# Optimization experiments

Measured on AMD Instinct MI355X. Metric: run time of the kernel, lower is better.

The kernel has to match this reference:

```python
import jax, jax.numpy as jnp
import numpy as np

B, N, D, OUT = 8, 65536, 128, 256
PARENT_IDX, BLOCK_START = 6, 7
relu = jax.nn.relu

def _w(key, fi, fo):
    return jax.random.normal(key, (fi, fo), dtype=jnp.float32) / np.sqrt(fi).astype(np.float32)

def setup_inputs() -> dict:
    key = jax.random.key(0)
    ks = jax.random.split(key, 16)
    feat = jax.random.normal(ks[0], (B, N, 6), dtype=jnp.float32)
    # parent index of each node, local to its batch's node axis
    pidx = jax.random.randint(ks[1], (B, N), 0, N).astype(jnp.float32)
    # block_start == 1 marks root nodes (parent feature is zeroed there)
    root = jnp.zeros((B, N), jnp.float32).at[:, 0].set(1.0)
    data = jnp.concatenate([feat, pidx[..., None], root[..., None]], axis=-1)
    z = lambda d: jnp.zeros((d,), jnp.float32)
    return {
        'data': data,
        'W1_0': _w(ks[2], 6, D),     'b1_0': z(D), 'W1_1': _w(ks[3], D, D), 'b1_1': z(D),
        'W2_0': _w(ks[4], 2 * D, D), 'b2_0': z(D), 'W2_1': _w(ks[5], D, D), 'b2_1': z(D),
        'W3_0': _w(ks[6], 2 * D, D), 'b3_0': z(D), 'W3_1': _w(ks[7], D, D), 'b3_1': z(D),
        'W4_0': _w(ks[8], 2 * D, D), 'b4_0': z(D), 'W4_1': _w(ks[9], D, D), 'b4_1': z(D),
        'Wfc': _w(ks[10], D, OUT),   'bfc': z(OUT),
    }

def reference(data, W1_0, b1_0, W1_1, b1_1, W2_0, b2_0, W2_1, b2_1,
              W3_0, b3_0, W3_1, b3_1, W4_0, b4_0, W4_1, b4_1, Wfc, bfc):
    pidx = jax.lax.stop_gradient(data[..., PARENT_IDX]).astype(jnp.int32)  # [B,N]
    root = jax.lax.stop_gradient(data[..., BLOCK_START]) == 1.0            # [B,N]

    def gather_parent(f):
        # [B,N,D] -> parent-node features, hard-coded to 0 at root nodes
        p = jnp.take_along_axis(f, pidx[:, :, None], axis=1)
        return jnp.where(root[:, :, None], 0.0, p)

    def res_block(f, W0, b0, W1, b1):
        h = jnp.concatenate([f, gather_parent(f)], axis=-1)  # [B,N,2D]
        h = relu(h @ W0 + b0) @ W1 + b1                      # mlp_dolastrelu=False
        return relu(h + f)

    x = data[..., :6]                        # ind_keep for in_feat_len == 6
    f1 = relu(x @ W1_0 + b1_0) @ W1_1 + b1_1 # nodewise_mlp1
    f2 = res_block(f1, W2_0, b2_0, W2_1, b2_1)
    f3 = res_block(f2, W3_0, b3_0, W3_1, b3_1)
    f4 = res_block(f3, W4_0, b4_0, W4_1, b4_1)
    return f4 @ Wfc + bfc                    # [B,N,256] occupancy logits
```

## Files before the change

kernel.cpp:

```cpp
#include <hip/hip_runtime.h>
#include <hip/hip_bf16.h>


typedef __bf16 bf16;
typedef bf16 bf16x8 __attribute__((ext_vector_type(8)));
typedef bf16 bf16x4 __attribute__((ext_vector_type(4)));
typedef float f32x4 __attribute__((ext_vector_type(4)));

#define MFMA16(a, b, c) __builtin_amdgcn_mfma_f32_16x16x32_bf16((a), (b), (c), 0, 0, 0)

#define BAR_LGKM() asm volatile("s_waitcnt lgkmcnt(0)\ns_barrier" ::: "memory")
#define BAR_VM(N) asm volatile("s_waitcnt vmcnt(" #N ")\ns_barrier" ::: "memory")

#define ZB    0
#define W10T  128
#define W11T  4224
#define W20T  20608
#define W21T  53376
#define W30T  69760
#define W31T  102528
#define W40T  118912
#define W41T  151680
#define WFCT  168064
#define PREP_TOTAL 200832
#define FA_BYTE  524288
#define F_STRIDE 134221824
#define FB_BYTE  (FA_BYTE + F_STRIDE)
#define PT_BYTE  (FA_BYTE + 2 * F_STRIDE)
#define ZROW_IDX 524288

__device__ __forceinline__ void gload16(const void* g, void* l) {
  __builtin_amdgcn_global_load_lds(
      (__attribute__((address_space(1))) void*)(g),
      (__attribute__((address_space(3))) void*)(l), 16, 0, 0);
}

__global__ void prep_kernel(const float* __restrict__ W1_0, const float* __restrict__ W1_1,
                            const float* __restrict__ W2_0, const float* __restrict__ W2_1,
                            const float* __restrict__ W3_0, const float* __restrict__ W3_1,
                            const float* __restrict__ W4_0, const float* __restrict__ W4_1,
                            const float* __restrict__ Wfc, bf16* __restrict__ wsb) {
  int i = blockIdx.x * 256 + threadIdx.x;
  if (i < 128) { wsb[ZB + i] = (bf16)0.0f; return; }
  i -= 128;
  if (i < 4096) { int n = i >> 5, k = i & 31;
    wsb[W10T + i] = (bf16)((k < 6) ? W1_0[k * 128 + n] : 0.0f); return; }
  i -= 4096;
  if (i < 16384) { int n = i >> 7, k = i & 127; wsb[W11T + i] = (bf16)W1_1[k * 128 + n]; return; }
  i -= 16384;
  if (i < 32768) { int n = i >> 8, k = i & 255; wsb[W20T + i] = (bf16)W2_0[k * 128 + n]; return; }
  i -= 32768;
  if (i < 16384) { int n = i >> 7, k = i & 127; wsb[W21T + i] = (bf16)W2_1[k * 128 + n]; return; }
  i -= 16384;
  if (i < 32768) { int n = i >> 8, k = i & 255; wsb[W30T + i] = (bf16)W3_0[k * 128 + n]; return; }
  i -= 32768;
  if (i < 16384) { int n = i >> 7, k = i & 127; wsb[W31T + i] = (bf16)W3_1[k * 128 + n]; return; }
  i -= 16384;
  if (i < 32768) { int n = i >> 8, k = i & 255; wsb[W40T + i] = (bf16)W4_0[k * 128 + n]; return; }
  i -= 32768;
  if (i < 16384) { int n = i >> 7, k = i & 127; wsb[W41T + i] = (bf16)W4_1[k * 128 + n]; return; }
  i -= 16384;
  if (i < 32768) { int n = i >> 7, k = i & 127; wsb[WFCT + i] = (bf16)Wfc[k * 256 + n]; return; }
}

__global__ void pidx_kernel(const float* __restrict__ data, int* __restrict__ partab,
                            bf16* __restrict__ fA, bf16* __restrict__ fB) {
  int m = blockIdx.x * 256 + threadIdx.x;
  float2 pr = *(const float2*)(data + (long)m * 8 + 6);
  partab[m] = (pr.y == 1.0f) ? ZROW_IDX : ((m & ~65535) + (int)pr.x);
  if (m < 128) {
    fA[(long)ZROW_IDX * 128 + m] = (bf16)0.0f;
    fB[(long)ZROW_IDX * 128 + m] = (bf16)0.0f;
  }
}

__device__ __forceinline__ void stage_tile(const bf16* __restrict__ f_in,
                                           const int* __restrict__ partab, long mt0,
                                           char* dst, int tid) {
  const int wv = tid >> 6;
  int par[8];
#pragma unroll
  for (int r = 0; r < 8; ++r) par[r] = partab[mt0 + r * 8 + (tid >> 5)];
#pragma unroll
  for (int r = 0; r < 8; ++r) {
    int row = r * 8 + (tid >> 5);
    int gp = tid & 31;
    int g = (gp & 8) | ((gp & 7) ^ (row & 7));
    const bf16* base = (gp < 16) ? (f_in + (mt0 + row) * 128) : (f_in + (long)par[r] * 128);
    gload16(base + g * 8, dst + (r * 256 + wv * 64) * 16);
  }
}

__device__ __forceinline__ void stage_ftile(const bf16* __restrict__ f_in, long mt0,
                                            char* dst, int tid) {
  const int wv = tid >> 6;
#pragma unroll
  for (int r = 0; r < 4; ++r) {
    int G = r * 256 + tid, row = G >> 4, gl = G & 15;
    int g = (gl & 8) | ((gl & 7) ^ (row & 7));
    gload16(f_in + (mt0 + row) * 128 + g * 8, dst + (r * 256 + wv * 64) * 16);
  }
}

__global__ __launch_bounds__(256, 3) void stage1_kernel(
    const float* __restrict__ data, const bf16* __restrict__ w0t, const float* __restrict__ b0,
    const bf16* __restrict__ w1t, const float* __restrict__ b1, bf16* __restrict__ f_out) {
  __shared__ alignas(128) char Hb[2][16384];

  const int tid = threadIdx.x;
  const int lane = tid & 63, wv = tid >> 6;
  const int lr = lane & 15, lq = lane >> 4;
  const long brow = (long)blockIdx.x * 512;
  const int n0 = wv * 32;

  bf16x8 w0f[2];
#pragma unroll
  for (int nf = 0; nf < 2; ++nf)
    w0f[nf] = *(const bf16x8*)(w0t + (long)(n0 + nf * 16 + lr) * 32 + lq * 8);
  bf16x8 w1f[4][2];
#pragma unroll
  for (int kc = 0; kc < 4; ++kc)
#pragma unroll
    for (int nf = 0; nf < 2; ++nf)
      w1f[kc][nf] = *(const bf16x8*)(w1t + (long)(n0 + nf * 16 + lr) * 128 + kc * 32 + lq * 8);
  f32x4 b0v[2], b1v[2];
#pragma unroll
  for (int nf = 0; nf < 2; ++nf) {
    b0v[nf] = *(const f32x4*)(b0 + n0 + nf * 16 + lq * 4);
    b1v[nf] = *(const f32x4*)(b1 + n0 + nf * 16 + lq * 4);
  }

  float4 xlo[4], xhi[4];
  if (lq == 0) {
#pragma unroll
    for (int mf = 0; mf < 4; ++mf) {
      const float* dp = data + (brow + mf * 16 + lr) * 8;
      xlo[mf] = *(const float4*)dp;
      xhi[mf] = *(const float4*)(dp + 4);
    }
  }

#pragma unroll 1
  for (int t = 0; t < 8; ++t) {
    bf16x8 xa[4];
#pragma unroll
    for (int mf = 0; mf < 4; ++mf) {
#pragma unroll
      for (int j = 0; j < 8; ++j) xa[mf][j] = (bf16)0.0f;
      if (lq == 0) {
#pragma unroll
        for (int j = 0; j < 4; ++j) xa[mf][j] = (bf16)xlo[mf][j];
        xa[mf][4] = (bf16)xhi[mf][0];
        xa[mf][5] = (bf16)xhi[mf][1];
      }
    }
    if (lq == 0) {
      long nb = brow + (long)((t < 7) ? t + 1 : 7) * 64;
#pragma unroll
      for (int mf = 0; mf < 4; ++mf) {
        const float* dp = data + (nb + mf * 16 + lr) * 8;
        xlo[mf] = *(const float4*)dp;
        xhi[mf] = *(const float4*)(dp + 4);
      }
    }

    f32x4 acc[4][2];
#pragma unroll
    for (int mf = 0; mf < 4; ++mf)
#pragma unroll
      for (int nf = 0; nf < 2; ++nf) acc[mf][nf] = b0v[nf];
#pragma unroll
    for (int mf = 0; mf < 4; ++mf)
#pragma unroll
      for (int nf = 0; nf < 2; ++nf) acc[mf][nf] = MFMA16(w0f[nf], xa[mf], acc[mf][nf]);

    char* H = Hb[t & 1];
#pragma unroll
    for (int mf = 0; mf < 4; ++mf)
#pragma unroll
      for (int nf = 0; nf < 2; ++nf) {
        int row = mf * 16 + lr, nc = n0 + nf * 16 + lq * 4;
        bf16x4 p;
#pragma unroll
        for (int j = 0; j < 4; ++j) p[j] = (bf16)fmaxf(acc[mf][nf][j], 0.0f);
        int g = nc >> 3, gp = (g & 8) | ((g & 7) ^ (row & 7));
        *(bf16x4*)(H + row * 256 + gp * 16 + (nc & 7) * 2) = p;
      }
    BAR_LGKM();

    f32x4 acc2[4][2];
#pragma unroll
    for (int mf = 0; mf < 4; ++mf)
#pragma unroll
      for (int nf = 0; nf < 2; ++nf) acc2[mf][nf] = b1v[nf];
#pragma unroll
    for (int kc = 0; kc < 4; ++kc) {
      bf16x8 a[4];
#pragma unroll
      for (int mf = 0; mf < 4; ++mf) {
        int row = mf * 16 + lr, g = kc * 4 + lq;
        int gp = (g & 8) | ((g & 7) ^ (row & 7));
        a[mf] = *(const bf16x8*)(H + row * 256 + gp * 16);
      }
#pragma unroll
      for (int mf = 0; mf < 4; ++mf)
#pragma unroll
        for (int nf = 0; nf < 2; ++nf) acc2[mf][nf] = MFMA16(w1f[kc][nf], a[mf], acc2[mf][nf]);
    }
    BAR_LGKM();

#pragma unroll
    for (int mf = 0; mf < 4; ++mf)
#pragma unroll
      for (int nf = 0; nf < 2; ++nf) {
        int row = mf * 16 + lr, nc = n0 + nf * 16 + lq * 4;
        bf16x4 p;
#pragma unroll
        for (int j = 0; j < 4; ++j) p[j] = (bf16)acc2[mf][nf][j];
        int g = nc >> 3, gp = (g & 8) | ((g & 7) ^ (row & 7));
        *(bf16x4*)(H + row * 256 + gp * 16 + (nc & 7) * 2) = p;
      }
    BAR_LGKM();

    long mt0 = brow + (long)t * 64;
#pragma unroll
    for (int r = 0; r < 4; ++r) {
      int G = r * 256 + tid, row = G >> 4, gl = G & 15;
      int gp = (gl & 8) | ((gl & 7) ^ (row & 7));
      bf16x8 v = *(const bf16x8*)(H + row * 256 + gp * 16);
      *(bf16x8*)(f_out + (mt0 + row) * 128 + gl * 8) = v;
    }
  }
}

__global__ __launch_bounds__(256, 2) void resblock_kernel(
    const bf16* __restrict__ f_in, const bf16* __restrict__ w0t, const float* __restrict__ b0,
    const bf16* __restrict__ w1t, const float* __restrict__ b1,
    const int* __restrict__ partab, bf16* __restrict__ f_out) {
  __shared__ alignas(128) char At[2][32768];

  const int tid = threadIdx.x;
  const int lane = tid & 63, wv = tid >> 6;
  const int lr = lane & 15, lq = lane >> 4;
  const long brow = (long)blockIdx.x * 1024;
  const int n0 = wv * 32;

  bf16x8 w0f[8][2];
#pragma unroll
  for (int kc = 0; kc < 8; ++kc)
#pragma unroll
    for (int nf = 0; nf < 2; ++nf)
      w0f[kc][nf] = *(const bf16x8*)(w0t + (long)(n0 + nf * 16 + lr) * 256 + kc * 32 + lq * 8);
  bf16x8 w1f[4][2];
#pragma unroll
  for (int kc = 0; kc < 4; ++kc)
#pragma unroll
    for (int nf = 0; nf < 2; ++nf)
      w1f[kc][nf] = *(const bf16x8*)(w1t + (long)(n0 + nf * 16 + lr) * 128 + kc * 32 + lq * 8);
  f32x4 b0v[2], b1v[2];
#pragma unroll
  for (int nf = 0; nf < 2; ++nf) {
    b0v[nf] = *(const f32x4*)(b0 + n0 + nf * 16 + lq * 4);
    b1v[nf] = *(const f32x4*)(b1 + n0 + nf * 16 + lq * 4);
  }

  stage_tile(f_in, partab, brow, At[0], tid);

#pragma unroll 1
  for (int t = 0; t < 16; ++t) {
    stage_tile(f_in, partab, brow + (long)((t < 15) ? t + 1 : 15) * 64, At[(t + 1) & 1], tid);
    if (t == 0) { BAR_VM(16); } else { BAR_VM(20); }
    char* A = At[t & 1];

    f32x4 acc[4][2];
#pragma unroll
    for (int mf = 0; mf < 4; ++mf)
#pragma unroll
      for (int nf = 0; nf < 2; ++nf) acc[mf][nf] = b0v[nf];
#pragma unroll
    for (int kc = 0; kc < 8; ++kc) {
      bf16x8 a[4];
#pragma unroll
      for (int mf = 0; mf < 4; ++mf) {
        int row = mf * 16 + lr, g = kc * 4 + lq;
        int gp = (g & 24) | ((g & 7) ^ (row & 7));
        a[mf] = *(const bf16x8*)(A + row * 512 + gp * 16);
      }
#pragma unroll
      for (int mf = 0; mf < 4; ++mf)
#pragma unroll
        for (int nf = 0; nf < 2; ++nf) acc[mf][nf] = MFMA16(w0f[kc][nf], a[mf], acc[mf][nf]);
    }
    BAR_LGKM();

#pragma unroll
    for (int mf = 0; mf < 4; ++mf)
#pragma unroll
      for (int nf = 0; nf < 2; ++nf) {
        int row = mf * 16 + lr, nc = n0 + nf * 16 + lq * 4;
        bf16x4 p;
#pragma unroll
        for (int j = 0; j < 4; ++j) p[j] = (bf16)fmaxf(acc[mf][nf][j], 0.0f);
        int g = nc >> 3, gp = (g & 8) | ((g & 7) ^ (row & 7));
        *(bf16x4*)(A + row * 512 + 256 + gp * 16 + (nc & 7) * 2) = p;
      }
    f32x4 acc2[4][2];
#pragma unroll
    for (int mf = 0; mf < 4; ++mf)
#pragma unroll
      for (int nf = 0; nf < 2; ++nf) {
        int row = mf * 16 + lr, nc = n0 + nf * 16 + lq * 4;
        int g = nc >> 3, gp = (g & 8) | ((g & 7) ^ (row & 7));
        bf16x4 res = *(const bf16x4*)(A + row * 512 + gp * 16 + (nc & 7) * 2);
#pragma unroll
        for (int j = 0; j < 4; ++j) acc2[mf][nf][j] = b1v[nf][j] + (float)res[j];
      }
    BAR_LGKM();

#pragma unroll
    for (int kc = 0; kc < 4; ++kc) {
      bf16x8 a[4];
#pragma unroll
      for (int mf = 0; mf < 4; ++mf) {
        int row = mf * 16 + lr, g = kc * 4 + lq;
        int gp = (g & 8) | ((g & 7) ^ (row & 7));
        a[mf] = *(const bf16x8*)(A + row * 512 + 256 + gp * 16);
      }
#pragma unroll
      for (int mf = 0; mf < 4; ++mf)
#pragma unroll
        for (int nf = 0; nf < 2; ++nf) acc2[mf][nf] = MFMA16(w1f[kc][nf], a[mf], acc2[mf][nf]);
    }
#pragma unroll
    for (int mf = 0; mf < 4; ++mf)
#pragma unroll
      for (int nf = 0; nf < 2; ++nf) {
        int row = mf * 16 + lr, nc = n0 + nf * 16 + lq * 4;
        bf16x4 p;
#pragma unroll
        for (int j = 0; j < 4; ++j) p[j] = (bf16)fmaxf(acc2[mf][nf][j], 0.0f);
        int g = nc >> 3, gp = (g & 8) | ((g & 7) ^ (row & 7));
        *(bf16x4*)(A + row * 512 + gp * 16 + (nc & 7) * 2) = p;
      }
    BAR_LGKM();

    bf16x8 v[4];
#pragma unroll
    for (int r = 0; r < 4; ++r) {
      int G = r * 256 + tid, row = G >> 4, gl = G & 15;
      int gp = (gl & 8) | ((gl & 7) ^ (row & 7));
      v[r] = *(const bf16x8*)(A + row * 512 + gp * 16);
    }
    BAR_LGKM();
    long mt0 = brow + (long)t * 64;
#pragma unroll
    for (int r = 0; r < 4; ++r) {
      int G = r * 256 + tid, row = G >> 4, gl = G & 15;
      *(bf16x8*)(f_out + (mt0 + row) * 128 + gl * 8) = v[r];
    }
  }
}

__global__ __launch_bounds__(256, 2) void fc_kernel(
    const bf16* __restrict__ f_in, const bf16* __restrict__ wt,
    const float* __restrict__ bias, float* __restrict__ out) {
  __shared__ alignas(128) char Ft[2][16384];

  const int tid = threadIdx.x;
  const int lane = tid & 63, wv = tid >> 6;
  const int lr = lane & 15, lq = lane >> 4;
  const long brow = (long)blockIdx.x * 512;
  const int c0 = wv * 64;

  bf16x8 wf[4][4];
#pragma unroll
  for (int kc = 0; kc < 4; ++kc)
#pragma unroll
    for (int nf = 0; nf < 4; ++nf)
      wf[kc][nf] = *(const bf16x8*)(wt + (long)(c0 + nf * 16 + lr) * 128 + kc * 32 + lq * 8);
  f32x4 bv[4];
#pragma unroll
  for (int nf = 0; nf < 4; ++nf) bv[nf] = *(const f32x4*)(bias + c0 + nf * 16 + lq * 4);

  stage_ftile(f_in, brow, Ft[0], tid);

#pragma unroll 1
  for (int t = 0; t < 8; ++t) {
    stage_ftile(f_in, brow + (long)((t < 7) ? t + 1 : 7) * 64, Ft[(t + 1) & 1], tid);
    if (t == 0) { BAR_VM(4); } else { BAR_VM(20); }
    char* F = Ft[t & 1];

    f32x4 acc[4][4];
#pragma unroll
    for (int mf = 0; mf < 4; ++mf)
#pragma unroll
      for (int nf = 0; nf < 4; ++nf) acc[mf][nf] = bv[nf];
#pragma unroll
    for (int kc = 0; kc < 4; ++kc) {
      bf16x8 a[4];
#pragma unroll
      for (int mf = 0; mf < 4; ++mf) {
        int row = mf * 16 + lr, g = kc * 4 + lq;
        int gp = (g & 8) | ((g & 7) ^ (row & 7));
        a[mf] = *(const bf16x8*)(F + row * 256 + gp * 16);
      }
#pragma unroll
      for (int mf = 0; mf < 4; ++mf)
#pragma unroll
        for (int nf = 0; nf < 4; ++nf) acc[mf][nf] = MFMA16(wf[kc][nf], a[mf], acc[mf][nf]);
    }
    BAR_LGKM();

    long mt0 = brow + (long)t * 64;
#pragma unroll
    for (int mf = 0; mf < 4; ++mf)
#pragma unroll
      for (int nf = 0; nf < 4; ++nf) {
        long row = mt0 + mf * 16 + lr;
        int col = c0 + nf * 16 + lq * 4;
        *(f32x4*)(out + row * 256 + col) = acc[mf][nf];
      }
  }
}

extern "C" void kernel_launch(void* const* d_in, const int* in_sizes, int n_in,
                              void* d_out, int out_size, void* d_ws, size_t ws_size,
                              hipStream_t stream) {
  const float* data = (const float*)d_in[0];
  const float* W1_0 = (const float*)d_in[1];
  const float* b1_0 = (const float*)d_in[2];
  const float* W1_1 = (const float*)d_in[3];
  const float* b1_1 = (const float*)d_in[4];
  const float* W2_0 = (const float*)d_in[5];
  const float* b2_0 = (const float*)d_in[6];
  const float* W2_1 = (const float*)d_in[7];
  const float* b2_1 = (const float*)d_in[8];
  const float* W3_0 = (const float*)d_in[9];
  const float* b3_0 = (const float*)d_in[10];
  const float* W3_1 = (const float*)d_in[11];
  const float* b3_1 = (const float*)d_in[12];
  const float* W4_0 = (const float*)d_in[13];
  const float* b4_0 = (const float*)d_in[14];
  const float* W4_1 = (const float*)d_in[15];
  const float* b4_1 = (const float*)d_in[16];
  const float* Wfc = (const float*)d_in[17];
  const float* bfc = (const float*)d_in[18];

  bf16* wsb = (bf16*)d_ws;
  bf16* fA = (bf16*)((char*)d_ws + FA_BYTE);
  bf16* fB = (bf16*)((char*)d_ws + FB_BYTE);
  int* partab = (int*)((char*)d_ws + PT_BYTE);

  prep_kernel<<<(PREP_TOTAL + 255) / 256, 256, 0, stream>>>(W1_0, W1_1, W2_0, W2_1, W3_0, W3_1,
                                                            W4_0, W4_1, Wfc, wsb);
  pidx_kernel<<<2048, 256, 0, stream>>>(data, partab, fA, fB);
  stage1_kernel<<<1024, 256, 0, stream>>>(data, wsb + W10T, b1_0, wsb + W11T, b1_1, fA);
  resblock_kernel<<<512, 256, 0, stream>>>(fA, wsb + W20T, b2_0, wsb + W21T, b2_1, partab, fB);
  resblock_kernel<<<512, 256, 0, stream>>>(fB, wsb + W30T, b3_0, wsb + W31T, b3_1, partab, fA);
  resblock_kernel<<<512, 256, 0, stream>>>(fA, wsb + W40T, b4_0, wsb + W41T, b4_1, partab, fB);
  fc_kernel<<<1024, 256, 0, stream>>>(fB, wsb + WFCT, bfc, (float*)d_out);
}
```

Measured before the change: 427.5 us.

## Fuse final FC projection into last residual block kernel

The last residual block now takes a template flag that makes it run the 128->256 output projection directly from the bf16 tile held in shared memory and write fp32 logits, instead of storing f4 to global memory and launching a separate FC kernel. This removes one kernel launch and the global write and reread of the final feature map. In exchange, the fused kernel reloads FC weight fragments from global/L2 for every tile in two halves to limit register pressure. The wait count on the async-load barrier is also changed to account for the different outstanding load pattern.

After: 512.0 us. 19.8% more time.

```diff
diff --git a/kernel.cpp b/kernel.cpp
--- a/kernel.cpp
+++ b/kernel.cpp
@@ -91,17 +91,6 @@
   }
 }
 
-__device__ __forceinline__ void stage_ftile(const bf16* __restrict__ f_in, long mt0,
-                                            char* dst, int tid) {
-  const int wv = tid >> 6;
-#pragma unroll
-  for (int r = 0; r < 4; ++r) {
-    int G = r * 256 + tid, row = G >> 4, gl = G & 15;
-    int g = (gl & 8) | ((gl & 7) ^ (row & 7));
-    gload16(f_in + (mt0 + row) * 128 + g * 8, dst + (r * 256 + wv * 64) * 16);
-  }
-}
-
 __global__ __launch_bounds__(256, 3) void stage1_kernel(
     const float* __restrict__ data, const bf16* __restrict__ w0t, const float* __restrict__ b0,
     const bf16* __restrict__ w1t, const float* __restrict__ b1, bf16* __restrict__ f_out) {
@@ -233,10 +222,13 @@
   }
 }
 
+template <bool FUSE_FC>
 __global__ __launch_bounds__(256, 2) void resblock_kernel(
     const bf16* __restrict__ f_in, const bf16* __restrict__ w0t, const float* __restrict__ b0,
     const bf16* __restrict__ w1t, const float* __restrict__ b1,
-    const int* __restrict__ partab, bf16* __restrict__ f_out) {
+    const int* __restrict__ partab, bf16* __restrict__ f_out,
+    const bf16* __restrict__ wfct, const float* __restrict__ bfc,
+    float* __restrict__ out) {
   __shared__ alignas(128) char At[2][32768];
 
   const int tid = threadIdx.x;
@@ -244,6 +236,7 @@
   const int lr = lane & 15, lq = lane >> 4;
   const long brow = (long)blockIdx.x * 1024;
   const int n0 = wv * 32;
+  const int c0 = wv * 64;
 
   bf16x8 w0f[8][2];
 #pragma unroll
@@ -263,13 +256,18 @@
     b0v[nf] = *(const f32x4*)(b0 + n0 + nf * 16 + lq * 4);
     b1v[nf] = *(const f32x4*)(b1 + n0 + nf * 16 + lq * 4);
   }
+  f32x4 bfcv[4];
+  if (FUSE_FC) {
+#pragma unroll
+    for (int nf = 0; nf < 4; ++nf) bfcv[nf] = *(const f32x4*)(bfc + c0 + nf * 16 + lq * 4);
+  }
 
   stage_tile(f_in, partab, brow, At[0], tid);
 
 #pragma unroll 1
   for (int t = 0; t < 16; ++t) {
     stage_tile(f_in, partab, brow + (long)((t < 15) ? t + 1 : 15) * 64, At[(t + 1) & 1], tid);
-    if (t == 0) { BAR_VM(16); } else { BAR_VM(20); }
+    if (t == 0) { BAR_VM(16); } else if (FUSE_FC) { BAR_VM(16); } else { BAR_VM(20); }
     char* A = At[t & 1];
 
     f32x4 acc[4][2];
@@ -344,82 +342,62 @@
       }
     BAR_LGKM();
 
-    bf16x8 v[4];
-#pragma unroll
-    for (int r = 0; r < 4; ++r) {
-      int G = r * 256 + tid, row = G >> 4, gl = G & 15;
-      int gp = (gl & 8) | ((gl & 7) ^ (row & 7));
-      v[r] = *(const bf16x8*)(A + row * 512 + gp * 16);
-    }
-    BAR_LGKM();
     long mt0 = brow + (long)t * 64;
-#pragma unroll
-    for (int r = 0; r < 4; ++r) {
-      int G = r * 256 + tid, row = G >> 4, gl = G & 15;
-      *(bf16x8*)(f_out + (mt0 + row) * 128 + gl * 8) = v[r];
-    }
-  }
-}
-
-__global__ __launch_bounds__(256, 2) void fc_kernel(
-    const bf16* __restrict__ f_in, const bf16* __restrict__ wt,
-    const float* __restrict__ bias, float* __restrict__ out) {
-  __shared__ alignas(128) char Ft[2][16384];
-
-  const int tid = threadIdx.x;
-  const int lane = tid & 63, wv = tid >> 6;
-  const int lr = lane & 15, lq = lane >> 4;
-  const long brow = (long)blockIdx.x * 512;
-  const int c0 = wv * 64;
-
-  bf16x8 wf[4][4];
-#pragma unroll
-  for (int kc = 0; kc < 4; ++kc)
-#pragma unroll
-    for (int nf = 0; nf < 4; ++nf)
-      wf[kc][nf] = *(const bf16x8*)(wt + (long)(c0 + nf * 16 + lr) * 128 + kc * 32 + lq * 8);
-  f32x4 bv[4];
-#pragma unroll
-  for (int nf = 0; nf < 4; ++nf) bv[nf] = *(const f32x4*)(bias + c0 + nf * 16 + lq * 4);
-
-  stage_ftile(f_in, brow, Ft[0], tid);
-
-#pragma unroll 1
-  for (int t = 0; t < 8; ++t) {
-    stage_ftile(f_in, brow + (long)((t < 7) ? t + 1 : 7) * 64, Ft[(t + 1) & 1], tid);
-    if (t == 0) { BAR_VM(4); } else { BAR_VM(20); }
-    char* F = Ft[t & 1];
-
-    f32x4 acc[4][4];
-#pragma unroll
-    for (int mf = 0; mf < 4; ++mf)
-#pragma unroll
-      for (int nf = 0; nf < 4; ++nf) acc[mf][nf] = bv[nf];
-#pragma unroll
-    for (int kc = 0; kc < 4; ++kc) {
-      bf16x8 a[4];
-#pragma unroll
-      for (int mf = 0; mf < 4; ++mf) {
-        int row = mf * 16 + lr, g = kc * 4 + lq;
-        int gp = (g & 8) | ((g & 7) ^ (row & 7));
-        a[mf] = *(const bf16x8*)(F + row * 256 + gp * 16);
-      }
-#pragma unroll
-      for (int mf = 0; mf < 4; ++mf)
-#pragma unroll
-        for (int nf = 0; nf < 4; ++nf) acc[mf][nf] = MFMA16(wf[kc][nf], a[mf], acc[mf][nf]);
-    }
-    BAR_LGKM();
-
-    long mt0 = brow + (long)t * 64;
-#pragma unroll
-    for (int mf = 0; mf < 4; ++mf)
-#pragma unroll
-      for (int nf = 0; nf < 4; ++nf) {
-        long row = mt0 + mf * 16 + lr;
-        int col = c0 + nf * 16 + lq * 4;
-        *(f32x4*)(out + row * 256 + col) = acc[mf][nf];
-      }
+    if (!FUSE_FC) {
+      bf16x8 v[4];
+#pragma unroll
+      for (int r = 0; r < 4; ++r) {
+        int G = r * 256 + tid, row = G >> 4, gl = G & 15;
+        int gp = (gl & 8) | ((gl & 7) ^ (row & 7));
+        v[r] = *(const bf16x8*)(A + row * 512 + gp * 16);
+      }
+      BAR_LGKM();
+#pragma unroll
+      for (int r = 0; r < 4; ++r) {
+        int G = r * 256 + tid, row = G >> 4, gl = G & 15;
+        *(bf16x8*)(f_out + (mt0 + row) * 128 + gl * 8) = v[r];
+      }
+    } else {
+#pragma unroll
+      for (int nh = 0; nh < 2; ++nh) {
+        bf16x8 wf2[4][2];
+#pragma unroll
+        for (int kc = 0; kc < 4; ++kc)
+#pragma unroll
+          for (int nf = 0; nf < 2; ++nf)
+            wf2[kc][nf] = *(const bf16x8*)(wfct + (long)(c0 + nh * 32 + nf * 16 + lr) * 128 +
+                                           kc * 32 + lq * 8);
+        f32x4 acc3[4][2];
+#pragma unroll
+        for (int mf = 0; mf < 4; ++mf)
+#pragma unroll
+          for (int nf = 0; nf < 2; ++nf) acc3[mf][nf] = bfcv[nh * 2 + nf];
+#pragma unroll
+        for (int kc = 0; kc < 4; ++kc) {
+          bf16x8 a[4];
+#pragma unroll
+          for (int mf = 0; mf < 4; ++mf) {
+            int row = mf * 16 + lr, g = kc * 4 + lq;
+            int gp = (g & 8) | ((g & 7) ^ (row & 7));
+            a[mf] = *(const bf16x8*)(A + row * 512 + gp * 16);
+          }
+#pragma unroll
+          for (int mf = 0; mf < 4; ++mf)
+#pragma unroll
+            for (int nf = 0; nf < 2; ++nf)
+              acc3[mf][nf] = MFMA16(wf2[kc][nf], a[mf], acc3[mf][nf]);
+        }
+#pragma unroll
+        for (int mf = 0; mf < 4; ++mf)
+#pragma unroll
+          for (int nf = 0; nf < 2; ++nf) {
+            long row = mt0 + mf * 16 + lr;
+            int col = c0 + nh * 32 + nf * 16 + lq * 4;
+            *(f32x4*)(out + row * 256 + col) = acc3[mf][nf];
+          }
+      }
+      BAR_LGKM();
+    }
   }
 }
 
@@ -455,8 +433,11 @@
                                                             W4_0, W4_1, Wfc, wsb);
   pidx_kernel<<<2048, 256, 0, stream>>>(data, partab, fA, fB);
   stage1_kernel<<<1024, 256, 0, stream>>>(data, wsb + W10T, b1_0, wsb + W11T, b1_1, fA);
-  resblock_kernel<<<512, 256, 0, stream>>>(fA, wsb + W20T, b2_0, wsb + W21T, b2_1, partab, fB);
-  resblock_kernel<<<512, 256, 0, stream>>>(fB, wsb + W30T, b3_0, wsb + W31T, b3_1, partab, fA);
-  resblock_kernel<<<512, 256, 0, stream>>>(fA, wsb + W40T, b4_0, wsb + W41T, b4_1, partab, fB);
-  fc_kernel<<<1024, 256, 0, stream>>>(fB, wsb + WFCT, bfc, (float*)d_out);
-}
+  resblock_kernel<false><<<512, 256, 0, stream>>>(fA, wsb + W20T, b2_0, wsb + W21T, b2_1,
+                                                  partab, fB, nullptr, nullptr, nullptr);
+  resblock_kernel<false><<<512, 256, 0, stream>>>(fB, wsb + W30T, b3_0, wsb + W31T, b3_1,
+                                                  partab, fA, nullptr, nullptr, nullptr);
+  resblock_kernel<true><<<512, 256, 0, stream>>>(fA, wsb + W40T, b4_0, wsb + W41T, b4_1,
+                                                 partab, nullptr, wsb + WFCT, bfc,
+                                                 (float*)d_out);
+}
```

## Write outputs directly from registers, prefetch parent indices, drop LDS staging in fc

Applied to the files above, without the earlier changes.

Stage1 and the resblock now store results straight from MFMA accumulators to global memory with bf16x4 writes, skipping the LDS round trip and its barriers. The resblock moves its hidden activations into a separate LDS buffer so the input tile is not overwritten, and it prefetches parent indices one tile ahead so the gather loads no longer wait on the index load. The fc kernel reads A fragments directly from global memory instead of staging them through double-buffered LDS. In exchange, global stores become narrower and less coalesced, the resblock uses more LDS per block, and fc loses its prefetch overlap.

Result: slower. 583.3 us (+36.5%).

```diff
diff --git a/kernel.cpp b/kernel.cpp
--- a/kernel.cpp
+++ b/kernel.cpp
@@ -74,13 +74,9 @@
   }
 }
 
-__device__ __forceinline__ void stage_tile(const bf16* __restrict__ f_in,
-                                           const int* __restrict__ partab, long mt0,
-                                           char* dst, int tid) {
+__device__ __forceinline__ void stage_tile(const bf16* __restrict__ f_in, const int* par,
+                                           long mt0, char* dst, int tid) {
   const int wv = tid >> 6;
-  int par[8];
-#pragma unroll
-  for (int r = 0; r < 8; ++r) par[r] = partab[mt0 + r * 8 + (tid >> 5)];
 #pragma unroll
   for (int r = 0; r < 8; ++r) {
     int row = r * 8 + (tid >> 5);
@@ -91,17 +87,6 @@
   }
 }
 
-__device__ __forceinline__ void stage_ftile(const bf16* __restrict__ f_in, long mt0,
-                                            char* dst, int tid) {
-  const int wv = tid >> 6;
-#pragma unroll
-  for (int r = 0; r < 4; ++r) {
-    int G = r * 256 + tid, row = G >> 4, gl = G & 15;
-    int g = (gl & 8) | ((gl & 7) ^ (row & 7));
-    gload16(f_in + (mt0 + row) * 128 + g * 8, dst + (r * 256 + wv * 64) * 16);
-  }
-}
-
 __global__ __launch_bounds__(256, 3) void stage1_kernel(
     const float* __restrict__ data, const bf16* __restrict__ w0t, const float* __restrict__ b0,
     const bf16* __restrict__ w1t, const float* __restrict__ b1, bf16* __restrict__ f_out) {
@@ -207,8 +192,8 @@
 #pragma unroll
         for (int nf = 0; nf < 2; ++nf) acc2[mf][nf] = MFMA16(w1f[kc][nf], a[mf], acc2[mf][nf]);
     }
-    BAR_LGKM();
-
+
+    long mt0 = brow + (long)t * 64;
 #pragma unroll
     for (int mf = 0; mf < 4; ++mf)
 #pragma unroll
@@ -217,19 +202,8 @@
         bf16x4 p;
 #pragma unroll
         for (int j = 0; j < 4; ++j) p[j] = (bf16)acc2[mf][nf][j];
-        int g = nc >> 3, gp = (g & 8) | ((g & 7) ^ (row & 7));
-        *(bf16x4*)(H + row * 256 + gp * 16 + (nc & 7) * 2) = p;
-      }
-    BAR_LGKM();
-
-    long mt0 = brow + (long)t * 64;
-#pragma unroll
-    for (int r = 0; r < 4; ++r) {
-      int G = r * 256 + tid, row = G >> 4, gl = G & 15;
-      int gp = (gl & 8) | ((gl & 7) ^ (row & 7));
-      bf16x8 v = *(const bf16x8*)(H + row * 256 + gp * 16);
-      *(bf16x8*)(f_out + (mt0 + row) * 128 + gl * 8) = v;
-    }
+        *(bf16x4*)(f_out + (mt0 + row) * 128 + nc) = p;
+      }
   }
 }
 
@@ -238,6 +212,7 @@
     const bf16* __restrict__ w1t, const float* __restrict__ b1,
     const int* __restrict__ partab, bf16* __restrict__ f_out) {
   __shared__ alignas(128) char At[2][32768];
+  __shared__ alignas(128) char Hl[16384];
 
   const int tid = threadIdx.x;
   const int lane = tid & 63, wv = tid >> 6;
@@ -264,12 +239,22 @@
     b1v[nf] = *(const f32x4*)(b1 + n0 + nf * 16 + lq * 4);
   }
 
-  stage_tile(f_in, partab, brow, At[0], tid);
+  int par0[8], par_s[8], par_n[8];
+#pragma unroll
+  for (int r = 0; r < 8; ++r) par0[r] = partab[brow + r * 8 + (tid >> 5)];
+  stage_tile(f_in, par0, brow, At[0], tid);
+#pragma unroll
+  for (int r = 0; r < 8; ++r) par_s[r] = partab[brow + 64 + r * 8 + (tid >> 5)];
 
 #pragma unroll 1
   for (int t = 0; t < 16; ++t) {
-    stage_tile(f_in, partab, brow + (long)((t < 15) ? t + 1 : 15) * 64, At[(t + 1) & 1], tid);
-    if (t == 0) { BAR_VM(16); } else { BAR_VM(20); }
+    stage_tile(f_in, par_s, brow + (long)((t < 15) ? t + 1 : 15) * 64, At[(t + 1) & 1], tid);
+    {
+      long pb = brow + (long)((t < 14) ? t + 2 : 15) * 64;
+#pragma unroll
+      for (int r = 0; r < 8; ++r) par_n[r] = partab[pb + r * 8 + (tid >> 5)];
+    }
+    BAR_VM(16);
     char* A = At[t & 1];
 
     f32x4 acc[4][2];
@@ -291,7 +276,6 @@
 #pragma unroll
         for (int nf = 0; nf < 2; ++nf) acc[mf][nf] = MFMA16(w0f[kc][nf], a[mf], acc[mf][nf]);
     }
-    BAR_LGKM();
 
 #pragma unroll
     for (int mf = 0; mf < 4; ++mf)
@@ -302,7 +286,7 @@
 #pragma unroll
         for (int j = 0; j < 4; ++j) p[j] = (bf16)fmaxf(acc[mf][nf][j], 0.0f);
         int g = nc >> 3, gp = (g & 8) | ((g & 7) ^ (row & 7));
-        *(bf16x4*)(A + row * 512 + 256 + gp * 16 + (nc & 7) * 2) = p;
+        *(bf16x4*)(Hl + row * 256 + gp * 16 + (nc & 7) * 2) = p;
       }
     f32x4 acc2[4][2];
 #pragma unroll
@@ -324,13 +308,15 @@
       for (int mf = 0; mf < 4; ++mf) {
         int row = mf * 16 + lr, g = kc * 4 + lq;
         int gp = (g & 8) | ((g & 7) ^ (row & 7));
-        a[mf] = *(const bf16x8*)(A + row * 512 + 256 + gp * 16);
+        a[mf] = *(const bf16x8*)(Hl + row * 256 + gp * 16);
       }
 #pragma unroll
       for (int mf = 0; mf < 4; ++mf)
 #pragma unroll
         for (int nf = 0; nf < 2; ++nf) acc2[mf][nf] = MFMA16(w1f[kc][nf], a[mf], acc2[mf][nf]);
     }
+
+    long mt0 = brow + (long)t * 64;
 #pragma unroll
     for (int mf = 0; mf < 4; ++mf)
 #pragma unroll
@@ -339,33 +325,16 @@
         bf16x4 p;
 #pragma unroll
         for (int j = 0; j < 4; ++j) p[j] = (bf16)fmaxf(acc2[mf][nf][j], 0.0f);
-        int g = nc >> 3, gp = (g & 8) | ((g & 7) ^ (row & 7));
-        *(bf16x4*)(A + row * 512 + gp * 16 + (nc & 7) * 2) = p;
-      }
-    BAR_LGKM();
-
-    bf16x8 v[4];
-#pragma unroll
-    for (int r = 0; r < 4; ++r) {
-      int G = r * 256 + tid, row = G >> 4, gl = G & 15;
-      int gp = (gl & 8) | ((gl & 7) ^ (row & 7));
-      v[r] = *(const bf16x8*)(A + row * 512 + gp * 16);
-    }
-    BAR_LGKM();
-    long mt0 = brow + (long)t * 64;
-#pragma unroll
-    for (int r = 0; r < 4; ++r) {
-      int G = r * 256 + tid, row = G >> 4, gl = G & 15;
-      *(bf16x8*)(f_out + (mt0 + row) * 128 + gl * 8) = v[r];
-    }
+        *(bf16x4*)(f_out + (mt0 + row) * 128 + nc) = p;
+      }
+#pragma unroll
+    for (int r = 0; r < 8; ++r) par_s[r] = par_n[r];
   }
 }
 
 __global__ __launch_bounds__(256, 2) void fc_kernel(
     const bf16* __restrict__ f_in, const bf16* __restrict__ wt,
     const float* __restrict__ bias, float* __restrict__ out) {
-  __shared__ alignas(128) char Ft[2][16384];
-
   const int tid = threadIdx.x;
   const int lane = tid & 63, wv = tid >> 6;
   const int lr = lane & 15, lq = lane >> 4;
@@ -382,13 +351,15 @@
 #pragma unroll
   for (int nf = 0; nf < 4; ++nf) bv[nf] = *(const f32x4*)(bias + c0 + nf * 16 + lq * 4);
 
-  stage_ftile(f_in, brow, Ft[0], tid);
-
 #pragma unroll 1
   for (int t = 0; t < 8; ++t) {
-    stage_ftile(f_in, brow + (long)((t < 7) ? t + 1 : 7) * 64, Ft[(t + 1) & 1], tid);
-    if (t == 0) { BAR_VM(4); } else { BAR_VM(20); }
-    char* F = Ft[t & 1];
+    long mt0 = brow + (long)t * 64;
+    bf16x8 a[4][4];
+#pragma unroll
+    for (int kc = 0; kc < 4; ++kc)
+#pragma unroll
+      for (int mf = 0; mf < 4; ++mf)
+        a[kc][mf] = *(const bf16x8*)(f_in + (mt0 + mf * 16 + lr) * 128 + kc * 32 + lq * 8);
 
     f32x4 acc[4][4];
 #pragma unroll
@@ -396,22 +367,12 @@
 #pragma unroll
       for (int nf = 0; nf < 4; ++nf) acc[mf][nf] = bv[nf];
 #pragma unroll
-    for (int kc = 0; kc < 4; ++kc) {
-      bf16x8 a[4];
-#pragma unroll
-      for (int mf = 0; mf < 4; ++mf) {
-        int row = mf * 16 + lr, g = kc * 4 + lq;
-        int gp = (g & 8) | ((g & 7) ^ (row & 7));
-        a[mf] = *(const bf16x8*)(F + row * 256 + gp * 16);
-      }
+    for (int kc = 0; kc < 4; ++kc)
 #pragma unroll
       for (int mf = 0; mf < 4; ++mf)
 #pragma unroll
-        for (int nf = 0; nf < 4; ++nf) acc[mf][nf] = MFMA16(wf[kc][nf], a[mf], acc[mf][nf]);
-    }
-    BAR_LGKM();
-
-    long mt0 = brow + (long)t * 64;
+        for (int nf = 0; nf < 4; ++nf) acc[mf][nf] = MFMA16(wf[kc][nf], a[kc][mf], acc[mf][nf]);
+
 #pragma unroll
     for (int mf = 0; mf < 4; ++mf)
 #pragma unroll
```

## Load parent-row operands straight from global into registers, staging only own rows in LDS

Applied to the files above, without the earlier changes.

The resblock kernel no longer stages the gathered parent half of the concatenated [f, parent] tile through LDS. Each lane now loads its parent-row MFMA fragments directly from global memory into registers. The own-feature tile is double-buffered in a smaller LDS region, and the hidden activation gets its own buffer. This halves LDS traffic and footprint per tile and drops one barrier. In exchange the parent gathers are synchronous per-lane loads issued inside the iteration rather than prefetched asynchronously, so their latency may be exposed, and register pressure rises.

New measurement: 518.0 us. +21.2%, slower.

```diff
diff --git a/kernel.cpp b/kernel.cpp
--- a/kernel.cpp
+++ b/kernel.cpp
@@ -74,23 +74,6 @@
   }
 }
 
-__device__ __forceinline__ void stage_tile(const bf16* __restrict__ f_in,
-                                           const int* __restrict__ partab, long mt0,
-                                           char* dst, int tid) {
-  const int wv = tid >> 6;
-  int par[8];
-#pragma unroll
-  for (int r = 0; r < 8; ++r) par[r] = partab[mt0 + r * 8 + (tid >> 5)];
-#pragma unroll
-  for (int r = 0; r < 8; ++r) {
-    int row = r * 8 + (tid >> 5);
-    int gp = tid & 31;
-    int g = (gp & 8) | ((gp & 7) ^ (row & 7));
-    const bf16* base = (gp < 16) ? (f_in + (mt0 + row) * 128) : (f_in + (long)par[r] * 128);
-    gload16(base + g * 8, dst + (r * 256 + wv * 64) * 16);
-  }
-}
-
 __device__ __forceinline__ void stage_ftile(const bf16* __restrict__ f_in, long mt0,
                                             char* dst, int tid) {
   const int wv = tid >> 6;
@@ -237,7 +220,8 @@
     const bf16* __restrict__ f_in, const bf16* __restrict__ w0t, const float* __restrict__ b0,
     const bf16* __restrict__ w1t, const float* __restrict__ b1,
     const int* __restrict__ partab, bf16* __restrict__ f_out) {
-  __shared__ alignas(128) char At[2][32768];
+  __shared__ alignas(128) char At[2][16384];
+  __shared__ alignas(128) char Hl[16384];
 
   const int tid = threadIdx.x;
   const int lane = tid & 63, wv = tid >> 6;
@@ -264,13 +248,24 @@
     b1v[nf] = *(const f32x4*)(b1 + n0 + nf * 16 + lq * 4);
   }
 
-  stage_tile(f_in, partab, brow, At[0], tid);
+  stage_ftile(f_in, brow, At[0], tid);
 
 #pragma unroll 1
   for (int t = 0; t < 16; ++t) {
-    stage_tile(f_in, partab, brow + (long)((t < 15) ? t + 1 : 15) * 64, At[(t + 1) & 1], tid);
-    if (t == 0) { BAR_VM(16); } else { BAR_VM(20); }
+    stage_ftile(f_in, brow + (long)((t < 15) ? t + 1 : 15) * 64, At[(t + 1) & 1], tid);
+    BAR_VM(4);
     char* A = At[t & 1];
+    long mt0 = brow + (long)t * 64;
+
+    int pidxv[4];
+#pragma unroll
+    for (int mf = 0; mf < 4; ++mf) pidxv[mf] = partab[mt0 + mf * 16 + lr];
+    bf16x8 pa[4][4];
+#pragma unroll
+    for (int kc2 = 0; kc2 < 4; ++kc2)
+#pragma unroll
+      for (int mf = 0; mf < 4; ++mf)
+        pa[kc2][mf] = *(const bf16x8*)(f_in + (long)pidxv[mf] * 128 + kc2 * 32 + lq * 8);
 
     f32x4 acc[4][2];
 #pragma unroll
@@ -278,20 +273,26 @@
 #pragma unroll
       for (int nf = 0; nf < 2; ++nf) acc[mf][nf] = b0v[nf];
 #pragma unroll
-    for (int kc = 0; kc < 8; ++kc) {
+    for (int kc = 0; kc < 4; ++kc) {
       bf16x8 a[4];
 #pragma unroll
       for (int mf = 0; mf < 4; ++mf) {
         int row = mf * 16 + lr, g = kc * 4 + lq;
-        int gp = (g & 24) | ((g & 7) ^ (row & 7));
-        a[mf] = *(const bf16x8*)(A + row * 512 + gp * 16);
+        int gp = (g & 8) | ((g & 7) ^ (row & 7));
+        a[mf] = *(const bf16x8*)(A + row * 256 + gp * 16);
       }
 #pragma unroll
       for (int mf = 0; mf < 4; ++mf)
 #pragma unroll
         for (int nf = 0; nf < 2; ++nf) acc[mf][nf] = MFMA16(w0f[kc][nf], a[mf], acc[mf][nf]);
     }
-    BAR_LGKM();
+#pragma unroll
+    for (int kc2 = 0; kc2 < 4; ++kc2)
+#pragma unroll
+      for (int mf = 0; mf < 4; ++mf)
+#pragma unroll
+        for (int nf = 0; nf < 2; ++nf)
+          acc[mf][nf] = MFMA16(w0f[4 + kc2][nf], pa[kc2][mf], acc[mf][nf]);
 
 #pragma unroll
     for (int mf = 0; mf < 4; ++mf)
@@ -302,7 +303,7 @@
 #pragma unroll
         for (int j = 0; j < 4; ++j) p[j] = (bf16)fmaxf(acc[mf][nf][j], 0.0f);
         int g = nc >> 3, gp = (g & 8) | ((g & 7) ^ (row & 7));
-        *(bf16x4*)(A + row * 512 + 256 + gp * 16 + (nc & 7) * 2) = p;
+        *(bf16x4*)(Hl + row * 256 + gp * 16 + (nc & 7) * 2) = p;
       }
     f32x4 acc2[4][2];
 #pragma unroll
@@ -311,7 +312,7 @@
       for (int nf = 0; nf < 2; ++nf) {
         int row = mf * 16 + lr, nc = n0 + nf * 16 + lq * 4;
         int g = nc >> 3, gp = (g & 8) | ((g & 7) ^ (row & 7));
-        bf16x4 res = *(const bf16x4*)(A + row * 512 + gp * 16 + (nc & 7) * 2);
+        bf16x4 res = *(const bf16x4*)(A + row * 256 + gp * 16 + (nc & 7) * 2);
 #pragma unroll
         for (int j = 0; j < 4; ++j) acc2[mf][nf][j] = b1v[nf][j] + (float)res[j];
       }
@@ -324,7 +325,7 @@
       for (int mf = 0; mf < 4; ++mf) {
         int row = mf * 16 + lr, g = kc * 4 + lq;
         int gp = (g & 8) | ((g & 7) ^ (row & 7));
-        a[mf] = *(const bf16x8*)(A + row * 512 + 256 + gp * 16);
+        a[mf] = *(const bf16x8*)(Hl + row * 256 + gp * 16);
       }
 #pragma unroll
       for (int mf = 0; mf < 4; ++mf)
@@ -340,7 +341,7 @@
 #pragma unroll
         for (int j = 0; j < 4; ++j) p[j] = (bf16)fmaxf(acc2[mf][nf][j], 0.0f);
         int g = nc >> 3, gp = (g & 8) | ((g & 7) ^ (row & 7));
-        *(bf16x4*)(A + row * 512 + gp * 16 + (nc & 7) * 2) = p;
+        *(bf16x4*)(A + row * 256 + gp * 16 + (nc & 7) * 2) = p;
       }
     BAR_LGKM();
 
@@ -349,10 +350,9 @@
     for (int r = 0; r < 4; ++r) {
       int G = r * 256 + tid, row = G >> 4, gl = G & 15;
       int gp = (gl & 8) | ((gl & 7) ^ (row & 7));
-      v[r] = *(const bf16x8*)(A + row * 512 + gp * 16);
-    }
-    BAR_LGKM();
-    long mt0 = brow + (long)t * 64;
+      v[r] = *(const bf16x8*)(A + row * 256 + gp * 16);
+    }
+    BAR_LGKM();
 #pragma unroll
     for (int r = 0; r < 4; ++r) {
       int G = r * 256 + tid, row = G >> 4, gl = G & 15;
```
